# Kernel tuning notes

Hardware: AMD Instinct MI355X
Metric: run time of the kernel (lower is better)

The kernel has to match this reference:

```python
import jax, jax.numpy as jnp
import numpy as np

B, T, C, H = 4, 2048, 1024, 16
D = C // H  # head dim 64


def setup_inputs() -> dict:
    key = jax.random.key(0)
    ks = jax.random.split(key, 5)
    s = 1.0 / np.sqrt(C)
    return {
        "x": jax.random.normal(ks[0], (B, T, C), jnp.float32),
        "Wq": jax.random.normal(ks[1], (C, C), jnp.float32) * s,
        "bq": jnp.zeros((C,), jnp.float32),
        "Wk": jax.random.normal(ks[2], (C, C), jnp.float32) * s,
        "bk": jnp.zeros((C,), jnp.float32),
        "Wv": jax.random.normal(ks[3], (C, C), jnp.float32) * s,
        "bv": jnp.zeros((C,), jnp.float32),
        "Wp": jax.random.normal(ks[4], (C, C), jnp.float32) * s,
        "bp": jnp.zeros((C,), jnp.float32),
    }


def reference(x, Wq, bq, Wk, bk, Wv, bv, Wp, bp):
    # project and split heads: [B,T,C] -> [B,H,T,D]
    def heads(w, b):
        return (x @ w.T + b).reshape(B, T, H, D).transpose(0, 2, 1, 3)

    q = heads(Wq, bq)
    k = heads(Wk, bk)
    v = heads(Wv, bv)

    att = jnp.einsum("bhqd,bhkd->bhqk", q, k) * (1.0 / np.sqrt(D))
    causal = jnp.tril(jnp.ones((T, T), bool))  # [T,T]
    att = jnp.where(causal[None, None], att, -jnp.inf)
    att = jax.nn.softmax(att, axis=-1)
    # dropout prob is 0.0 -> identity
    y = jnp.einsum("bhqk,bhkd->bhqd", att, v)
    y = y.transpose(0, 2, 1, 3).reshape(B, T, C)
    return y @ Wp.T + bp
```

## Files before the change

### kernel.cpp

```cpp
#include <hip/hip_runtime.h>
#include <hip/hip_bf16.h>

#define BB 4
#define TT 2048
#define CC 1024
#define HH 16
#define DD 64
#define PSTR 80

typedef unsigned short u16;
typedef __attribute__((ext_vector_type(8))) short bf16x8;
typedef __attribute__((ext_vector_type(4))) float f32x4;

__device__ __forceinline__ float bf2f(u16 v) {
    union { unsigned u; float f; } c; c.u = ((unsigned)v) << 16; return c.f;
}
__device__ __forceinline__ u16 f2bf(float f) {
    union { float f; unsigned u; } c; c.f = f;
    unsigned u = c.u + 0x7fffu + ((c.u >> 16) & 1u);
    return (u16)(u >> 16);
}
__device__ __forceinline__ float scrub(float v) {
    v = fminf(fmaxf(v, -3.0e38f), 3.0e38f);
    return (v == v) ? v : 0.0f;
}
__device__ __forceinline__ float fast_exp2(float x) {
    float r;
    asm volatile("v_exp_f32 %0, %1\n\ts_nop 1" : "=v"(r) : "v"(x));
    return r;
}
__device__ __forceinline__ unsigned pack_bf16(unsigned b0, unsigned b1, unsigned sel) {
    unsigned d;
    asm("v_perm_b32 %0, %1, %2, %3" : "=v"(d) : "v"(b1), "v"(b0), "v"(sel));
    return d;
}
__device__ __forceinline__ void gload16(const u16* g, u16* l) {
    __builtin_amdgcn_global_load_lds(
        (const __attribute__((address_space(1))) void*)g,
        (__attribute__((address_space(3))) void*)l, 16, 0, 0);
}

__global__ void detect_dtype(const u16* __restrict__ x, int* __restrict__ flag) {
    __shared__ int cnt;
    if (threadIdx.x == 0) cnt = 0;
    __syncthreads();
    int local = 0;
    for (int i = 0; i < 16; i++) {
        u16 h = x[(threadIdx.x * 16 + i) * 2];
        int e = (h >> 7) & 0xFF;
        if (e >= 118 && e <= 132) local++;
    }
    atomicAdd(&cnt, local);
    __syncthreads();
    if (threadIdx.x == 0) *flag = (cnt >= 2048) ? 1 : 0;
}

struct CastArgs {
    const void* src[9];
    u16* dst[9];
    int blk_start[10];
    int n[9];
};
__global__ __launch_bounds__(256) void cast_all(CastArgs a, const int* __restrict__ flag) {
    int b = blockIdx.x;
    int s = 0;
    while (s < 8 && b >= a.blk_start[s + 1]) s++;
    int i0 = (b - a.blk_start[s]) * 2048 + threadIdx.x * 8;
    if (i0 + 8 > a.n[s]) return;
    if (*flag) {
        *(uint4*)&a.dst[s][i0] = *(const uint4*)&((const u16*)a.src[s])[i0];
    } else {
        const float* sp = (const float*)a.src[s];
        u16 tmp[8];
#pragma unroll
        for (int j = 0; j < 8; j++) tmp[j] = f2bf(sp[i0 + j]);
        *(uint4*)&a.dst[s][i0] = *(uint4*)tmp;
    }
}


template <int MODE>
__device__ __forceinline__ void gemm_core(
    const u16* __restrict__ X, const u16* __restrict__ W,
    u16* Als, u16* Bls, f32x4 (&acc)[4][4],
    int m0, int n0, int wave, int lane, int quad, int l16, int wm, int wn)
{
    int srow[4], sch[4];
#pragma unroll
    for (int c = 0; c < 4; c++) {
        srow[c] = wave * 32 + c * 8 + (lane >> 3);
        sch[c]  = (lane & 7) ^ (srow[c] & 7);
    }

    for (int k0 = 0; k0 < CC; k0 += 64) {
        __syncthreads();
#pragma unroll
        for (int c = 0; c < 4; c++) {
            gload16(&X[(size_t)(m0 + srow[c]) * CC + k0 + sch[c] * 8],
                    &Als[wave * 2048 + c * 512]);
            gload16(&W[(size_t)(n0 + srow[c]) * CC + k0 + sch[c] * 8],
                    &Bls[wave * 2048 + c * 512]);
        }
        __syncthreads();

#pragma unroll
        for (int kk = 0; kk < 2; kk++) {
            const int sw = ((kk * 4 + quad) ^ (l16 & 7)) * 8;
            bf16x8 a[4], b[4];
#pragma unroll
            for (int i = 0; i < 4; i++)
                a[i] = *(const bf16x8*)&Als[(wm + i * 16 + l16) * 64 + sw];
#pragma unroll
            for (int j = 0; j < 4; j++)
                b[j] = *(const bf16x8*)&Bls[(wn + j * 16 + l16) * 64 + sw];
#pragma unroll
            for (int i = 0; i < 4; i++)
#pragma unroll
                for (int j = 0; j < 4; j++)
                    acc[i][j] = __builtin_amdgcn_mfma_f32_16x16x32_bf16(
                        a[i], b[j], acc[i][j], 0, 0, 0);
        }
    }
}

__global__ __launch_bounds__(256) void gemm_qkv(
    const u16* __restrict__ X,
    const u16* __restrict__ Wq, const u16* __restrict__ Wk, const u16* __restrict__ Wv,
    const u16* __restrict__ bq, const u16* __restrict__ bk, const u16* __restrict__ bv,
    u16* __restrict__ Q, u16* __restrict__ K, u16* __restrict__ VT)
{
    __shared__ __align__(16) u16 Als[128 * 64];
    __shared__ __align__(16) u16 Bls[128 * 64];

    const int tid  = threadIdx.x;
    const int wave = tid >> 6;
    const int lane = tid & 63;
    const int quad = lane >> 4;
    const int l16  = lane & 15;
    const int m0   = blockIdx.x * 128;
    const int n0   = blockIdx.y * 128;
    const int z    = blockIdx.z;
    const int wm   = (wave >> 1) * 64;
    const int wn   = (wave & 1) * 64;

    const u16* W    = (z == 0) ? Wq : (z == 1) ? Wk : Wv;
    const u16* bias = (z == 0) ? bq : (z == 1) ? bk : bv;

    f32x4 acc[4][4];
#pragma unroll
    for (int i = 0; i < 4; i++)
#pragma unroll
        for (int j = 0; j < 4; j++) acc[i][j] = (f32x4)0.0f;

    gemm_core<0>(X, W, Als, Bls, acc, m0, n0, wave, lane, quad, l16, wm, wn);

    const float scale = (z == 0) ? 0.18033688f : 1.0f;
    u16* outp = (z == 0) ? Q : (z == 1) ? K : VT;

#pragma unroll
    for (int j = 0; j < 4; j++) {
        const int n = n0 + wn + j * 16 + l16;
        const float bvv = bf2f(bias[n]);
        const int hh = n >> 6, d = n & 63;
#pragma unroll
        for (int i = 0; i < 4; i++) {
#pragma unroll
            for (int r = 0; r < 4; r++) {
                const int m = m0 + wm + i * 16 + quad * 4 + r;
                const int bb = m >> 11, t = m & (TT - 1);
                const float val = scrub((acc[i][j][r] + bvv) * scale);
                size_t idx = (z < 2)
                    ? ((size_t)(bb * HH + hh) * TT + t) * DD + d
                    : ((size_t)(bb * HH + hh) * DD + d) * TT + t;
                outp[idx] = f2bf(val);
            }
        }
    }
}

__global__ __launch_bounds__(256) void gemm_proj(
    const u16* __restrict__ X, const u16* __restrict__ W,
    const u16* __restrict__ bias, void* __restrict__ out,
    const int* __restrict__ flag)
{
    __shared__ __align__(16) u16 Als[128 * 64];
    __shared__ __align__(16) u16 Bls[128 * 64];

    const int tid  = threadIdx.x;
    const int wave = tid >> 6;
    const int lane = tid & 63;
    const int quad = lane >> 4;
    const int l16  = lane & 15;
    const int m0   = blockIdx.x * 128;
    const int n0   = blockIdx.y * 128;
    const int wm   = (wave >> 1) * 64;
    const int wn   = (wave & 1) * 64;
    const int isbf = *flag;

    f32x4 acc[4][4];
#pragma unroll
    for (int i = 0; i < 4; i++)
#pragma unroll
        for (int j = 0; j < 4; j++) acc[i][j] = (f32x4)0.0f;

    gemm_core<1>(X, W, Als, Bls, acc, m0, n0, wave, lane, quad, l16, wm, wn);

#pragma unroll
    for (int j = 0; j < 4; j++) {
        const int n = n0 + wn + j * 16 + l16;
        const float bvv = bf2f(bias[n]);
#pragma unroll
        for (int i = 0; i < 4; i++) {
#pragma unroll
            for (int r = 0; r < 4; r++) {
                const int m = m0 + wm + i * 16 + quad * 4 + r;
                const float val = scrub(acc[i][j][r] + bvv);
                size_t idx = (size_t)m * CC + n;
                if (isbf) ((u16*)out)[idx] = f2bf(val);
                else      ((float*)out)[idx] = val;
            }
        }
    }
}

__global__ __launch_bounds__(256) void attn_kernel(
    const u16* __restrict__ Qg, const u16* __restrict__ Kg,
    const u16* __restrict__ VTg, u16* __restrict__ Yg)
{
    __shared__ __align__(16) u16 Qs[64 * 64];
    __shared__ __align__(16) u16 Ks[64 * 64];
    __shared__ __align__(16) u16 VTs[64 * 64];
    __shared__ __align__(16) u16 Ps[64 * PSTR];
    __shared__ float ls[64];

    const int tid  = threadIdx.x;
    const int wave = tid >> 6;
    const int lane = tid & 63;
    const int quad = lane >> 4;
    const int l16  = lane & 15;
    const int bh    = blockIdx.x;
    const int qtile = (TT / 64 - 1) - blockIdx.y;
    const int h = bh & (HH - 1);
    const int b = bh >> 4;
    const int q0 = qtile * 64;
    const unsigned perm_sel = 0x07060302u;

    int srow[2], sch[2];
#pragma unroll
    for (int c = 0; c < 2; c++) {
        srow[c] = wave * 16 + c * 8 + (lane >> 3);
        sch[c]  = (lane & 7) ^ (srow[c] & 7);
    }

    const u16* kp[2];
    const u16* vp[2];
#pragma unroll
    for (int c = 0; c < 2; c++) {
        kp[c] = Kg + (size_t)bh * TT * DD + (size_t)srow[c] * DD + sch[c] * 8;
        vp[c] = VTg + (size_t)bh * DD * TT + (size_t)srow[c] * TT + sch[c] * 8;
    }

#pragma unroll
    for (int c = 0; c < 2; c++)
        gload16(&Qg[((size_t)bh * TT + q0 + srow[c]) * DD + sch[c] * 8],
                &Qs[wave * 1024 + c * 512]);
    __syncthreads();
    bf16x8 qf[2];
#pragma unroll
    for (int ks = 0; ks < 2; ks++)
        qf[ks] = *(const bf16x8*)&Qs[(wave * 16 + l16) * 64 + ((ks * 4 + quad) ^ (l16 & 7)) * 8];

    f32x4 o_acc[4];
#pragma unroll
    for (int jt = 0; jt < 4; jt++) o_acc[jt] = (f32x4)0.0f;
    float lsum = 0.0f;

    const int qrow_g = q0 + wave * 16 + l16;
    const u16* psrow = &Ps[(wave * 16 + l16) * PSTR];

    for (int kv = 0; kv < qtile; kv++) {
        __syncthreads();
#pragma unroll
        for (int c = 0; c < 2; c++) {
            gload16(kp[c], &Ks[wave * 1024 + c * 512]);
            gload16(vp[c], &VTs[wave * 1024 + c * 512]);
            kp[c] += 64 * DD;
            vp[c] += 64;
        }
        __syncthreads();

        f32x4 st[4];
#pragma unroll
        for (int j = 0; j < 4; j++) st[j] = (f32x4)0.0f;
#pragma unroll
        for (int ks = 0; ks < 2; ks++) {
            const int rsw = ((ks * 4 + quad) ^ (l16 & 7)) * 8;
#pragma unroll
            for (int j = 0; j < 4; j++) {
                bf16x8 kf = *(const bf16x8*)&Ks[(j * 16 + l16) * 64 + rsw];
                st[j] = __builtin_amdgcn_mfma_f32_16x16x32_bf16(kf, qf[ks], st[j], 0, 0, 0);
            }
        }

#pragma unroll
        for (int j = 0; j < 4; j++) {
            float e0 = fast_exp2(st[j][0]);
            float e1 = fast_exp2(st[j][1]);
            float e2 = fast_exp2(st[j][2]);
            float e3 = fast_exp2(st[j][3]);
            lsum += (e0 + e1) + (e2 + e3);
            unsigned lo = pack_bf16(__float_as_uint(e0) + 0x8000u,
                                    __float_as_uint(e1) + 0x8000u, perm_sel);
            unsigned hi = pack_bf16(__float_as_uint(e2) + 0x8000u,
                                    __float_as_uint(e3) + 0x8000u, perm_sel);
            uint2 pk; pk.x = lo; pk.y = hi;
            *(uint2*)&psrow[j * 16 + quad * 4] = pk;
        }

#pragma unroll
        for (int ks = 0; ks < 2; ks++) {
            bf16x8 pf = *(const bf16x8*)&psrow[ks * 32 + quad * 8];
            const int rsw = ((ks * 4 + quad) ^ (l16 & 7)) * 8;
#pragma unroll
            for (int jt = 0; jt < 4; jt++) {
                bf16x8 vf = *(const bf16x8*)&VTs[(jt * 16 + l16) * 64 + rsw];
                o_acc[jt] = __builtin_amdgcn_mfma_f32_16x16x32_bf16(pf, vf, o_acc[jt], 0, 0, 0);
            }
        }
    }

    {
        __syncthreads();
#pragma unroll
        for (int c = 0; c < 2; c++) {
            gload16(kp[c], &Ks[wave * 1024 + c * 512]);
            gload16(vp[c], &VTs[wave * 1024 + c * 512]);
        }
        __syncthreads();

        f32x4 st[4];
#pragma unroll
        for (int j = 0; j < 4; j++) st[j] = (f32x4)0.0f;
#pragma unroll
        for (int ks = 0; ks < 2; ks++) {
            const int rsw = ((ks * 4 + quad) ^ (l16 & 7)) * 8;
#pragma unroll
            for (int j = 0; j < 4; j++) {
                bf16x8 kf = *(const bf16x8*)&Ks[(j * 16 + l16) * 64 + rsw];
                st[j] = __builtin_amdgcn_mfma_f32_16x16x32_bf16(kf, qf[ks], st[j], 0, 0, 0);
            }
        }

#pragma unroll
        for (int j = 0; j < 4; j++) {
            const int kc_base = q0 + j * 16 + quad * 4;
            float e[4];
#pragma unroll
            for (int r = 0; r < 4; r++) {
                float ev = fast_exp2(st[j][r]);
                if (kc_base + r > qrow_g) ev = 0.0f;
                e[r] = ev;
            }
            lsum += (e[0] + e[1]) + (e[2] + e[3]);
            unsigned lo = pack_bf16(__float_as_uint(e[0]) + 0x8000u,
                                    __float_as_uint(e[1]) + 0x8000u, perm_sel);
            unsigned hi = pack_bf16(__float_as_uint(e[2]) + 0x8000u,
                                    __float_as_uint(e[3]) + 0x8000u, perm_sel);
            uint2 pk; pk.x = lo; pk.y = hi;
            *(uint2*)&psrow[j * 16 + quad * 4] = pk;
        }

#pragma unroll
        for (int ks = 0; ks < 2; ks++) {
            bf16x8 pf = *(const bf16x8*)&psrow[ks * 32 + quad * 8];
            const int rsw = ((ks * 4 + quad) ^ (l16 & 7)) * 8;
#pragma unroll
            for (int jt = 0; jt < 4; jt++) {
                bf16x8 vf = *(const bf16x8*)&VTs[(jt * 16 + l16) * 64 + rsw];
                o_acc[jt] = __builtin_amdgcn_mfma_f32_16x16x32_bf16(pf, vf, o_acc[jt], 0, 0, 0);
            }
        }
    }

    lsum += __shfl_xor(lsum, 16, 64);
    lsum += __shfl_xor(lsum, 32, 64);
    ls[wave * 16 + l16] = lsum;

    float linv[4];
#pragma unroll
    for (int r = 0; r < 4; r++)
        linv[r] = 1.0f / fmaxf(ls[wave * 16 + quad * 4 + r], 1e-20f);

#pragma unroll
    for (int jt = 0; jt < 4; jt++) {
#pragma unroll
        for (int r = 0; r < 4; r++) {
            const int t = q0 + wave * 16 + quad * 4 + r;
            const int c = h * DD + jt * 16 + l16;
            Yg[((size_t)b * TT + t) * CC + c] = f2bf(scrub(o_acc[jt][r] * linv[r]));
        }
    }
}

extern "C" void kernel_launch(void* const* d_in, const int* in_sizes, int n_in,
                              void* d_out, int out_size, void* d_ws, size_t ws_size,
                              hipStream_t stream) {
    u16* w = (u16*)d_ws;
    int* flag = (int*)d_ws;
    size_t off = 128;
    const size_t NX = (size_t)BB * TT * CC;
    const size_t NW = (size_t)CC * CC;
    const size_t NB = CC;
    const size_t per = (size_t)BB * HH * TT * DD;

    u16* xb  = w + off; off += NX;
    u16* Wqb = w + off; off += NW;
    u16* Wkb = w + off; off += NW;
    u16* Wvb = w + off; off += NW;
    u16* Wpb = w + off; off += NW;
    u16* bqb = w + off; off += NB;
    u16* bkb = w + off; off += NB;
    u16* bvb = w + off; off += NB;
    u16* bpb = w + off; off += NB;
    u16* Q   = w + off; off += per;
    u16* K   = w + off; off += per;
    u16* VT  = w + off; off += per;
    u16* Y   = w + off; off += per;

    detect_dtype<<<1, 256, 0, stream>>>((const u16*)d_in[0], flag);

    CastArgs ca;
    const int srcmap[9] = {0, 1, 3, 5, 7, 2, 4, 6, 8};
    u16* dsts[9] = {xb, Wqb, Wkb, Wvb, Wpb, bqb, bkb, bvb, bpb};
    int ns[9] = {(int)NX, (int)NW, (int)NW, (int)NW, (int)NW,
                 (int)NB, (int)NB, (int)NB, (int)NB};
    int acc_blk = 0;
    for (int i = 0; i < 9; i++) {
        ca.src[i] = d_in[srcmap[i]];
        ca.dst[i] = dsts[i];
        ca.n[i]   = ns[i];
        ca.blk_start[i] = acc_blk;
        acc_blk += (ns[i] + 2047) / 2048;
    }
    ca.blk_start[9] = acc_blk;
    cast_all<<<acc_blk, 256, 0, stream>>>(ca, flag);

    gemm_qkv<<<dim3(64, 8, 3), 256, 0, stream>>>(xb, Wqb, Wkb, Wvb,
                                                 bqb, bkb, bvb, Q, K, VT);
    attn_kernel<<<dim3(BB * HH, TT / 64), 256, 0, stream>>>(Q, K, VT, Y);
    gemm_proj<<<dim3(64, 8), 256, 0, stream>>>(Y, Wpb, bpb, d_out, flag);
}
```

Measured before the change: 271.9 us.

## Enlarge attention query tile to 128 rows and vectorize GEMM epilogue stores

The attention kernel now processes 128 query rows per block (two 16-row groups per wave), so each K/V tile loaded into LDS serves twice as many queries. The diagonal handling is merged into the main loop with a masked flag. The GEMMs swap the MFMA operand order so each lane holds four consecutive output columns, which allows packed 8-byte bf16 and float4 stores and one vector bias load per lane. The scrub clamping is removed everywhere. Trade-offs are higher register and LDS use per block, half as many attention blocks, and no more NaN/Inf sanitization.

After: 261.6 us. -3.8%, faster.

```diff
diff --git a/kernel.cpp b/kernel.cpp
--- a/kernel.cpp
+++ b/kernel.cpp
@@ -20,19 +20,21 @@
     unsigned u = c.u + 0x7fffu + ((c.u >> 16) & 1u);
     return (u16)(u >> 16);
 }
-__device__ __forceinline__ float scrub(float v) {
-    v = fminf(fmaxf(v, -3.0e38f), 3.0e38f);
-    return (v == v) ? v : 0.0f;
-}
 __device__ __forceinline__ float fast_exp2(float x) {
     float r;
     asm volatile("v_exp_f32 %0, %1\n\ts_nop 1" : "=v"(r) : "v"(x));
     return r;
 }
-__device__ __forceinline__ unsigned pack_bf16(unsigned b0, unsigned b1, unsigned sel) {
+__device__ __forceinline__ unsigned pack_bf16(unsigned b0, unsigned b1) {
     unsigned d;
-    asm("v_perm_b32 %0, %1, %2, %3" : "=v"(d) : "v"(b1), "v"(b0), "v"(sel));
+    asm("v_perm_b32 %0, %1, %2, %3" : "=v"(d) : "v"(b1), "v"(b0), "v"(0x07060302u));
     return d;
+}
+__device__ __forceinline__ uint2 pack4(float v0, float v1, float v2, float v3) {
+    uint2 pk;
+    pk.x = pack_bf16(__float_as_uint(v0) + 0x8000u, __float_as_uint(v1) + 0x8000u);
+    pk.y = pack_bf16(__float_as_uint(v2) + 0x8000u, __float_as_uint(v3) + 0x8000u);
+    return pk;
 }
 __device__ __forceinline__ void gload16(const u16* g, u16* l) {
     __builtin_amdgcn_global_load_lds(
@@ -78,8 +80,6 @@
     }
 }
 
-
-template <int MODE>
 __device__ __forceinline__ void gemm_core(
     const u16* __restrict__ X, const u16* __restrict__ W,
     u16* Als, u16* Bls, f32x4 (&acc)[4][4],
@@ -118,7 +118,7 @@
 #pragma unroll
                 for (int j = 0; j < 4; j++)
                     acc[i][j] = __builtin_amdgcn_mfma_f32_16x16x32_bf16(
-                        a[i], b[j], acc[i][j], 0, 0, 0);
+                        b[j], a[i], acc[i][j], 0, 0, 0);
         }
     }
 }
@@ -152,27 +152,37 @@
 #pragma unroll
         for (int j = 0; j < 4; j++) acc[i][j] = (f32x4)0.0f;
 
-    gemm_core<0>(X, W, Als, Bls, acc, m0, n0, wave, lane, quad, l16, wm, wn);
+    gemm_core(X, W, Als, Bls, acc, m0, n0, wave, lane, quad, l16, wm, wn);
 
     const float scale = (z == 0) ? 0.18033688f : 1.0f;
     u16* outp = (z == 0) ? Q : (z == 1) ? K : VT;
 
 #pragma unroll
     for (int j = 0; j < 4; j++) {
-        const int n = n0 + wn + j * 16 + l16;
-        const float bvv = bf2f(bias[n]);
-        const int hh = n >> 6, d = n & 63;
+        const int n_base = n0 + wn + j * 16 + quad * 4;
+        union { uint2 u; u16 us[4]; } braw;
+        braw.u = *(const uint2*)&bias[n_base];
+        float bvv[4];
+#pragma unroll
+        for (int r = 0; r < 4; r++) bvv[r] = bf2f(braw.us[r]);
+        const int hh = n_base >> 6, d0 = n_base & 63;
 #pragma unroll
         for (int i = 0; i < 4; i++) {
-#pragma unroll
-            for (int r = 0; r < 4; r++) {
-                const int m = m0 + wm + i * 16 + quad * 4 + r;
-                const int bb = m >> 11, t = m & (TT - 1);
-                const float val = scrub((acc[i][j][r] + bvv) * scale);
-                size_t idx = (z < 2)
-                    ? ((size_t)(bb * HH + hh) * TT + t) * DD + d
-                    : ((size_t)(bb * HH + hh) * DD + d) * TT + t;
-                outp[idx] = f2bf(val);
+            const int m = m0 + wm + i * 16 + l16;
+            const int bb = m >> 11, t = m & (TT - 1);
+            float v0 = (acc[i][j][0] + bvv[0]) * scale;
+            float v1 = (acc[i][j][1] + bvv[1]) * scale;
+            float v2 = (acc[i][j][2] + bvv[2]) * scale;
+            float v3 = (acc[i][j][3] + bvv[3]) * scale;
+            if (z < 2) {
+                *(uint2*)&outp[((size_t)(bb * HH + hh) * TT + t) * DD + d0] =
+                    pack4(v0, v1, v2, v3);
+            } else {
+                const size_t base = (size_t)(bb * HH + hh) * DD * TT + t;
+                outp[base + (size_t)(d0 + 0) * TT] = f2bf(v0);
+                outp[base + (size_t)(d0 + 1) * TT] = f2bf(v1);
+                outp[base + (size_t)(d0 + 2) * TT] = f2bf(v2);
+                outp[base + (size_t)(d0 + 3) * TT] = f2bf(v3);
             }
         }
     }
@@ -203,21 +213,28 @@
 #pragma unroll
         for (int j = 0; j < 4; j++) acc[i][j] = (f32x4)0.0f;
 
-    gemm_core<1>(X, W, Als, Bls, acc, m0, n0, wave, lane, quad, l16, wm, wn);
+    gemm_core(X, W, Als, Bls, acc, m0, n0, wave, lane, quad, l16, wm, wn);
 
 #pragma unroll
     for (int j = 0; j < 4; j++) {
-        const int n = n0 + wn + j * 16 + l16;
-        const float bvv = bf2f(bias[n]);
+        const int n_base = n0 + wn + j * 16 + quad * 4;
+        union { uint2 u; u16 us[4]; } braw;
+        braw.u = *(const uint2*)&bias[n_base];
+        float bvv[4];
+#pragma unroll
+        for (int r = 0; r < 4; r++) bvv[r] = bf2f(braw.us[r]);
 #pragma unroll
         for (int i = 0; i < 4; i++) {
-#pragma unroll
-            for (int r = 0; r < 4; r++) {
-                const int m = m0 + wm + i * 16 + quad * 4 + r;
-                const float val = scrub(acc[i][j][r] + bvv);
-                size_t idx = (size_t)m * CC + n;
-                if (isbf) ((u16*)out)[idx] = f2bf(val);
-                else      ((float*)out)[idx] = val;
+            const int m = m0 + wm + i * 16 + l16;
+            float v0 = acc[i][j][0] + bvv[0];
+            float v1 = acc[i][j][1] + bvv[1];
+            float v2 = acc[i][j][2] + bvv[2];
+            float v3 = acc[i][j][3] + bvv[3];
+            if (isbf) {
+                *(uint2*)&((u16*)out)[(size_t)m * CC + n_base] = pack4(v0, v1, v2, v3);
+            } else {
+                float4 f; f.x = v0; f.y = v1; f.z = v2; f.w = v3;
+                *(float4*)&((float*)out)[(size_t)m * CC + n_base] = f;
             }
         }
     }
@@ -227,11 +244,11 @@
     const u16* __restrict__ Qg, const u16* __restrict__ Kg,
     const u16* __restrict__ VTg, u16* __restrict__ Yg)
 {
-    __shared__ __align__(16) u16 Qs[64 * 64];
+    __shared__ __align__(16) u16 Qs[128 * 64];
     __shared__ __align__(16) u16 Ks[64 * 64];
     __shared__ __align__(16) u16 VTs[64 * 64];
-    __shared__ __align__(16) u16 Ps[64 * PSTR];
-    __shared__ float ls[64];
+    __shared__ __align__(16) u16 Ps[128 * PSTR];
+    __shared__ float ls[128];
 
     const int tid  = threadIdx.x;
     const int wave = tid >> 6;
@@ -239,46 +256,48 @@
     const int quad = lane >> 4;
     const int l16  = lane & 15;
     const int bh    = blockIdx.x;
-    const int qtile = (TT / 64 - 1) - blockIdx.y;
+    const int qtile = (TT / 128 - 1) - blockIdx.y;
     const int h = bh & (HH - 1);
     const int b = bh >> 4;
-    const int q0 = qtile * 64;
-    const unsigned perm_sel = 0x07060302u;
-
-    int srow[2], sch[2];
-#pragma unroll
-    for (int c = 0; c < 2; c++) {
-        srow[c] = wave * 16 + c * 8 + (lane >> 3);
-        sch[c]  = (lane & 7) ^ (srow[c] & 7);
-    }
+    const int q0 = qtile * 128;
+
+    const int sch = (lane & 7) ^ (lane >> 3);
 
     const u16* kp[2];
     const u16* vp[2];
 #pragma unroll
     for (int c = 0; c < 2; c++) {
-        kp[c] = Kg + (size_t)bh * TT * DD + (size_t)srow[c] * DD + sch[c] * 8;
-        vp[c] = VTg + (size_t)bh * DD * TT + (size_t)srow[c] * TT + sch[c] * 8;
-    }
-
-#pragma unroll
-    for (int c = 0; c < 2; c++)
-        gload16(&Qg[((size_t)bh * TT + q0 + srow[c]) * DD + sch[c] * 8],
-                &Qs[wave * 1024 + c * 512]);
+        const int srow = wave * 16 + c * 8 + (lane >> 3);
+        kp[c] = Kg + (size_t)bh * TT * DD + (size_t)srow * DD + sch * 8;
+        vp[c] = VTg + (size_t)bh * DD * TT + (size_t)srow * TT + sch * 8;
+    }
+
+#pragma unroll
+    for (int c = 0; c < 4; c++) {
+        const int srow = wave * 32 + c * 8 + (lane >> 3);
+        gload16(&Qg[((size_t)bh * TT + q0 + srow) * DD + sch * 8],
+                &Qs[wave * 2048 + c * 512]);
+    }
     __syncthreads();
-    bf16x8 qf[2];
-#pragma unroll
-    for (int ks = 0; ks < 2; ks++)
-        qf[ks] = *(const bf16x8*)&Qs[(wave * 16 + l16) * 64 + ((ks * 4 + quad) ^ (l16 & 7)) * 8];
-
-    f32x4 o_acc[4];
-#pragma unroll
-    for (int jt = 0; jt < 4; jt++) o_acc[jt] = (f32x4)0.0f;
-    float lsum = 0.0f;
-
-    const int qrow_g = q0 + wave * 16 + l16;
-    const u16* psrow = &Ps[(wave * 16 + l16) * PSTR];
-
-    for (int kv = 0; kv < qtile; kv++) {
+    bf16x8 qf[2][2];
+#pragma unroll
+    for (int g = 0; g < 2; g++)
+#pragma unroll
+        for (int ks = 0; ks < 2; ks++)
+            qf[g][ks] = *(const bf16x8*)&Qs[(wave * 32 + g * 16 + l16) * 64 +
+                                            ((ks * 4 + quad) ^ (l16 & 7)) * 8];
+
+    f32x4 o_acc[2][4];
+#pragma unroll
+    for (int g = 0; g < 2; g++)
+#pragma unroll
+        for (int jt = 0; jt < 4; jt++) o_acc[g][jt] = (f32x4)0.0f;
+    float lsum[2] = {0.0f, 0.0f};
+
+    const int ntiles = 2 * qtile;
+
+    for (int kv = 0; kv < ntiles + 2; kv++) {
+        const bool masked = (kv >= ntiles);
         __syncthreads();
 #pragma unroll
         for (int c = 0; c < 2; c++) {
@@ -289,115 +308,91 @@
         }
         __syncthreads();
 
-        f32x4 st[4];
-#pragma unroll
-        for (int j = 0; j < 4; j++) st[j] = (f32x4)0.0f;
+        f32x4 st[2][4];
+#pragma unroll
+        for (int g = 0; g < 2; g++)
+#pragma unroll
+            for (int j = 0; j < 4; j++) st[g][j] = (f32x4)0.0f;
 #pragma unroll
         for (int ks = 0; ks < 2; ks++) {
             const int rsw = ((ks * 4 + quad) ^ (l16 & 7)) * 8;
 #pragma unroll
             for (int j = 0; j < 4; j++) {
                 bf16x8 kf = *(const bf16x8*)&Ks[(j * 16 + l16) * 64 + rsw];
-                st[j] = __builtin_amdgcn_mfma_f32_16x16x32_bf16(kf, qf[ks], st[j], 0, 0, 0);
-            }
-        }
-
-#pragma unroll
-        for (int j = 0; j < 4; j++) {
-            float e0 = fast_exp2(st[j][0]);
-            float e1 = fast_exp2(st[j][1]);
-            float e2 = fast_exp2(st[j][2]);
-            float e3 = fast_exp2(st[j][3]);
-            lsum += (e0 + e1) + (e2 + e3);
-            unsigned lo = pack_bf16(__float_as_uint(e0) + 0x8000u,
-                                    __float_as_uint(e1) + 0x8000u, perm_sel);
-            unsigned hi = pack_bf16(__float_as_uint(e2) + 0x8000u,
-                                    __float_as_uint(e3) + 0x8000u, perm_sel);
-            uint2 pk; pk.x = lo; pk.y = hi;
-            *(uint2*)&psrow[j * 16 + quad * 4] = pk;
-        }
-
-#pragma unroll
-        for (int ks = 0; ks < 2; ks++) {
-            bf16x8 pf = *(const bf16x8*)&psrow[ks * 32 + quad * 8];
-            const int rsw = ((ks * 4 + quad) ^ (l16 & 7)) * 8;
-#pragma unroll
-            for (int jt = 0; jt < 4; jt++) {
-                bf16x8 vf = *(const bf16x8*)&VTs[(jt * 16 + l16) * 64 + rsw];
-                o_acc[jt] = __builtin_amdgcn_mfma_f32_16x16x32_bf16(pf, vf, o_acc[jt], 0, 0, 0);
-            }
-        }
-    }
-
-    {
-        __syncthreads();
-#pragma unroll
-        for (int c = 0; c < 2; c++) {
-            gload16(kp[c], &Ks[wave * 1024 + c * 512]);
-            gload16(vp[c], &VTs[wave * 1024 + c * 512]);
-        }
-        __syncthreads();
-
-        f32x4 st[4];
-#pragma unroll
-        for (int j = 0; j < 4; j++) st[j] = (f32x4)0.0f;
-#pragma unroll
-        for (int ks = 0; ks < 2; ks++) {
-            const int rsw = ((ks * 4 + quad) ^ (l16 & 7)) * 8;
+#pragma unroll
+                for (int g = 0; g < 2; g++)
+                    st[g][j] = __builtin_amdgcn_mfma_f32_16x16x32_bf16(
+                        kf, qf[g][ks], st[g][j], 0, 0, 0);
+            }
+        }
+
+#pragma unroll
+        for (int g = 0; g < 2; g++) {
+            u16* psrow = &Ps[(wave * 32 + g * 16 + l16) * PSTR];
+            const int qrow = q0 + wave * 32 + g * 16 + l16;
+            float lp = 0.0f;
 #pragma unroll
             for (int j = 0; j < 4; j++) {
-                bf16x8 kf = *(const bf16x8*)&Ks[(j * 16 + l16) * 64 + rsw];
-                st[j] = __builtin_amdgcn_mfma_f32_16x16x32_bf16(kf, qf[ks], st[j], 0, 0, 0);
-            }
-        }
-
-#pragma unroll
-        for (int j = 0; j < 4; j++) {
-            const int kc_base = q0 + j * 16 + quad * 4;
-            float e[4];
+                float e0 = fast_exp2(st[g][j][0]);
+                float e1 = fast_exp2(st[g][j][1]);
+                float e2 = fast_exp2(st[g][j][2]);
+                float e3 = fast_exp2(st[g][j][3]);
+                if (masked) {
+                    const int kc = kv * 64 + j * 16 + quad * 4;
+                    if (kc + 0 > qrow) e0 = 0.0f;
+                    if (kc + 1 > qrow) e1 = 0.0f;
+                    if (kc + 2 > qrow) e2 = 0.0f;
+                    if (kc + 3 > qrow) e3 = 0.0f;
+                }
+                lp += (e0 + e1) + (e2 + e3);
+                uint2 pk;
+                pk.x = pack_bf16(__float_as_uint(e0) + 0x8000u,
+                                 __float_as_uint(e1) + 0x8000u);
+                pk.y = pack_bf16(__float_as_uint(e2) + 0x8000u,
+                                 __float_as_uint(e3) + 0x8000u);
+                *(uint2*)&psrow[j * 16 + quad * 4] = pk;
+            }
+            lsum[g] += lp;
+        }
+
+#pragma unroll
+        for (int g = 0; g < 2; g++) {
+#pragma unroll
+            for (int ks = 0; ks < 2; ks++) {
+                bf16x8 pf = *(const bf16x8*)&Ps[(wave * 32 + g * 16 + l16) * PSTR +
+                                                ks * 32 + quad * 8];
+                const int rsw = ((ks * 4 + quad) ^ (l16 & 7)) * 8;
+#pragma unroll
+                for (int jt = 0; jt < 4; jt++) {
+                    bf16x8 vf = *(const bf16x8*)&VTs[(jt * 16 + l16) * 64 + rsw];
+                    o_acc[g][jt] = __builtin_amdgcn_mfma_f32_16x16x32_bf16(
+                        pf, vf, o_acc[g][jt], 0, 0, 0);
+                }
+            }
+        }
+    }
+
+#pragma unroll
+    for (int g = 0; g < 2; g++) {
+        lsum[g] += __shfl_xor(lsum[g], 16, 64);
+        lsum[g] += __shfl_xor(lsum[g], 32, 64);
+        ls[wave * 32 + g * 16 + l16] = lsum[g];
+    }
+
+#pragma unroll
+    for (int g = 0; g < 2; g++) {
+        float linv[4];
+#pragma unroll
+        for (int r = 0; r < 4; r++)
+            linv[r] = 1.0f / fmaxf(ls[wave * 32 + g * 16 + quad * 4 + r], 1e-20f);
+#pragma unroll
+        for (int jt = 0; jt < 4; jt++) {
 #pragma unroll
             for (int r = 0; r < 4; r++) {
-                float ev = fast_exp2(st[j][r]);
-                if (kc_base + r > qrow_g) ev = 0.0f;
-                e[r] = ev;
-            }
-            lsum += (e[0] + e[1]) + (e[2] + e[3]);
-            unsigned lo = pack_bf16(__float_as_uint(e[0]) + 0x8000u,
-                                    __float_as_uint(e[1]) + 0x8000u, perm_sel);
-            unsigned hi = pack_bf16(__float_as_uint(e[2]) + 0x8000u,
-                                    __float_as_uint(e[3]) + 0x8000u, perm_sel);
-            uint2 pk; pk.x = lo; pk.y = hi;
-            *(uint2*)&psrow[j * 16 + quad * 4] = pk;
-        }
-
-#pragma unroll
-        for (int ks = 0; ks < 2; ks++) {
-            bf16x8 pf = *(const bf16x8*)&psrow[ks * 32 + quad * 8];
-            const int rsw = ((ks * 4 + quad) ^ (l16 & 7)) * 8;
-#pragma unroll
-            for (int jt = 0; jt < 4; jt++) {
-                bf16x8 vf = *(const bf16x8*)&VTs[(jt * 16 + l16) * 64 + rsw];
-                o_acc[jt] = __builtin_amdgcn_mfma_f32_16x16x32_bf16(pf, vf, o_acc[jt], 0, 0, 0);
-            }
-        }
-    }
-
-    lsum += __shfl_xor(lsum, 16, 64);
-    lsum += __shfl_xor(lsum, 32, 64);
-    ls[wave * 16 + l16] = lsum;
-
-    float linv[4];
-#pragma unroll
-    for (int r = 0; r < 4; r++)
-        linv[r] = 1.0f / fmaxf(ls[wave * 16 + quad * 4 + r], 1e-20f);
-
-#pragma unroll
-    for (int jt = 0; jt < 4; jt++) {
-#pragma unroll
-        for (int r = 0; r < 4; r++) {
-            const int t = q0 + wave * 16 + quad * 4 + r;
-            const int c = h * DD + jt * 16 + l16;
-            Yg[((size_t)b * TT + t) * CC + c] = f2bf(scrub(o_acc[jt][r] * linv[r]));
+                const int t = q0 + wave * 32 + g * 16 + quad * 4 + r;
+                const int c = h * DD + jt * 16 + l16;
+                Yg[((size_t)b * TT + t) * CC + c] = f2bf(o_acc[g][jt][r] * linv[r]);
+            }
         }
     }
 }
@@ -447,6 +442,6 @@
 
     gemm_qkv<<<dim3(64, 8, 3), 256, 0, stream>>>(xb, Wqb, Wkb, Wvb,
                                                  bqb, bkb, bvb, Q, K, VT);
-    attn_kernel<<<dim3(BB * HH, TT / 64), 256, 0, stream>>>(Q, K, VT, Y);
+    attn_kernel<<<dim3(BB * HH, TT / 128), 256, 0, stream>>>(Q, K, VT, Y);
     gemm_proj<<<dim3(64, 8), 256, 0, stream>>>(Y, Wpb, bpb, d_out, flag);
 }
```
